# Kernel optimization log

Measured on AMD Instinct MI355X. Metric: run time of the kernel, lower is better.

Reference implementation:

```python
import jax, jax.numpy as jnp
import numpy as np

EPS = 1e-5

def layer_norm(x, gamma, beta):
    mu = jnp.mean(x, axis=-1, keepdims=True)
    var = jnp.mean(jnp.square(x - mu), axis=-1, keepdims=True)
    return (x - mu) * jax.lax.rsqrt(var + EPS) * gamma + beta

def setup_inputs() -> dict:
    key = jax.random.key(0)
    ks = jax.random.split(key, 12)
    B, N, F, H, K = 32, 2048, 128, 256, 64
    A_hat = jax.random.uniform(ks[0], (B, N, N), dtype=jnp.float32) / N  # row-normalized-ish adjacency
    X = jax.random.normal(ks[1], (B, N, F), dtype=jnp.float32)
    def lin(k, din, dout):
        s = 1.0 / np.sqrt(din)
        k1, k2 = jax.random.split(k)
        W = jax.random.uniform(k1, (din, dout), minval=-s, maxval=s, dtype=jnp.float32)
        b = jax.random.uniform(k2, (dout,), minval=-s, maxval=s, dtype=jnp.float32)
        return W, b
    W1, b1 = lin(ks[2], F, H)
    W2, b2 = lin(ks[3], H, H)
    Wa, ba = lin(ks[4], H, K)
    Wl, bl = lin(ks[5], H, K)
    g1 = jnp.ones((H,), jnp.float32); beta1 = jnp.zeros((H,), jnp.float32)
    g2 = jnp.ones((H,), jnp.float32); beta2 = jnp.zeros((H,), jnp.float32)
    return {"A_hat": A_hat, "X": X, "W1": W1, "b1": b1, "g1": g1, "beta1": beta1,
            "W2": W2, "b2": b2, "g2": g2, "beta2": beta2,
            "Wa": Wa, "ba": ba, "Wl": Wl, "bl": bl}

def reference(A_hat, X, W1, b1, g1, beta1, W2, b2, g2, beta2, Wa, ba, Wl, bl):
    # Layer 1: aggregate -> linear -> LayerNorm -> ReLU (dropout is eval identity)
    H = jnp.einsum('bnm,bmf->bnf', A_hat, X)
    H = jnp.einsum('bnf,fh->bnh', H, W1) + b1
    H = jax.nn.relu(layer_norm(H, g1, beta1))
    # Layer 2
    H = jnp.einsum('bnm,bmh->bnh', A_hat, H)
    H = jnp.einsum('bnh,hk->bnk', H, W2) + b2
    H = jax.nn.relu(layer_norm(H, g2, beta2))
    # mean readout over nodes
    g = jnp.mean(H, axis=1)
    pred_arr_reg = g @ Wa + ba
    logits = g @ Wl + bl
    return (pred_arr_reg, logits)
```

## Files before the change

### kernel.cpp

```cpp
#include <hip/hip_runtime.h>
#include <hip/hip_bf16.h>

#define NN 2048

typedef __attribute__((ext_vector_type(4))) float f32x4;
typedef __attribute__((ext_vector_type(8))) short bf16x8;

__device__ __forceinline__ unsigned short f2bf(float f) {
  __hip_bfloat16 h = __float2bfloat16(f);
  return __builtin_bit_cast(unsigned short, h);
}
__device__ __forceinline__ unsigned int pk2(float a, float b) {
  return (unsigned int)f2bf(a) | ((unsigned int)f2bf(b) << 16);
}
__device__ __forceinline__ void gld_lds16(const void* g, void* l) {
  __builtin_amdgcn_global_load_lds(
      (const __attribute__((address_space(1))) unsigned int*)g,
      (__attribute__((address_space(3))) unsigned int*)l, 16, 0, 0);
}

__global__ void k_tr_cvt(const float* __restrict__ src, unsigned short* __restrict__ dst,
                         int R, int C) {
  int b = blockIdx.z;
  src += (size_t)b * R * C;
  dst += (size_t)b * R * C;
  __shared__ float tile[32][33];
  int r0 = blockIdx.x * 32, c0 = blockIdx.y * 32;
  int t = threadIdx.x;
  int r = t >> 3, c4 = (t & 7) << 2;
  float4 v = *(const float4*)(src + (size_t)(r0 + r) * C + c0 + c4);
  tile[r][c4 + 0] = v.x; tile[r][c4 + 1] = v.y; tile[r][c4 + 2] = v.z; tile[r][c4 + 3] = v.w;
  __syncthreads();
  ushort4 o;
  o.x = f2bf(tile[c4 + 0][r]); o.y = f2bf(tile[c4 + 1][r]);
  o.z = f2bf(tile[c4 + 2][r]); o.w = f2bf(tile[c4 + 3][r]);
  *(ushort4*)(dst + (size_t)(c0 + r) * R + r0 + c4) = o;
}

#define AGG_STEP(KT, AREGC, AREGN, CUR)                                        \
  {                                                                            \
    const int kt_ = (KT);                                                      \
    if (kt_ < NKT - 2) {                           \
      const float* p_ = apb + (size_t)(kt_ + 2) * 64;                          \
      _Pragma("unroll") for (int j = 0; j < 4; ++j)                            \
          AREGN[j] = ((const float4*)p_)[j];                                   \
    }                                                                          \
    if (kt_ < NKT - 1) {                                                       \
      _Pragma("unroll") for (int i = 0; i < NF; ++i) {        \
        int jj = i * 512 + t;                                                  \
        int n_ = jj >> 3, s_ = jj & 7, sp_ = s_ ^ (n_ & 7);                    \
        gld_lds16(BTb + (size_t)n_ * NN + (size_t)(kt_ + 1) * 64 + sp_ * 8,    \
                  &Bs[(CUR) ^ 1][(i * 512 + wid * 64) * 8]);                   \
      }                                                                        \
      _Pragma("unroll") for (int i = 0; i < 2; ++i) {     \
        uint4 w_;                                                              \
        w_.x = pk2(AREGC[2 * i].x, AREGC[2 * i].y);                            \
        w_.y = pk2(AREGC[2 * i].z, AREGC[2 * i].w);                            \
        w_.z = pk2(AREGC[2 * i + 1].x, AREGC[2 * i + 1].y);                    \
        w_.w = pk2(AREGC[2 * i + 1].z, AREGC[2 * i + 1].w);                    \
        int s_ = ak * 2 + i, sp_ = s_ ^ (ar & 7);                              \
        *(uint4*)&As[(CUR) ^ 1][(ar * 8 + sp_) * 8] = w_;                      \
      }                                                                        \
    }                                                                          \
    _Pragma("unroll") for (int kh = 0; kh < 2; ++kh) {                         \
      bf16x8 af[4], bfr[NF];                                                   \
      _Pragma("unroll") for (int mi = 0; mi < 4; ++mi) {                       \
        int row = wr * 64 + mi * 16 + lr;                                      \
        int sp_ = (kh * 4 + q) ^ (row & 7);                                    \
        af[mi] = *(const bf16x8*)&As[CUR][(row * 8 + sp_) * 8];                \
      }                                                                        \
      _Pragma("unroll") for (int ni = 0; ni < NF; ++ni) {                      \
        int brow = wc * WN + ni * 16 + lr;                                     \
        int sp_ = (kh * 4 + q) ^ (brow & 7);                                   \
        bfr[ni] = *(const bf16x8*)&Bs[CUR][(brow * 8 + sp_) * 8];              \
      }                                                                        \
      _Pragma("unroll") for (int mi = 0; mi < 4; ++mi)                         \
        _Pragma("unroll") for (int ni = 0; ni < NF; ++ni)                      \
          acc[mi][ni] = __builtin_amdgcn_mfma_f32_16x16x32_bf16(               \
              af[mi], bfr[ni], acc[mi][ni], 0, 0, 0);                          \
    }                                                                          \
    __syncthreads();                                                           \
  }

template <int NCOLS, int MODE>
__global__ __launch_bounds__(512, NCOLS == 128 ? 4 : 2) void k_agg_fused(
    const float* __restrict__ A, const unsigned short* __restrict__ BT,
    const unsigned short* __restrict__ WT, const float* __restrict__ bias,
    const float* __restrict__ gamma, const float* __restrict__ beta,
    unsigned short* __restrict__ HTout, float* __restrict__ gpart) {
  constexpr int WN = NCOLS / 4;
  constexpr int NF = NCOLS / 64;
  constexpr int NKT = NN / 64;
  constexpr int FIN = NCOLS;
  constexpr int NQT = FIN / 64;
  constexpr int NMB = NN / 128;

  __shared__ __align__(16) unsigned short As[2][128 * 64];
  __shared__ __align__(16) unsigned short Bs[2][NCOLS * 64];
  __shared__ float red[2][128][4];

  int L = blockIdx.x + gridDim.x * blockIdx.z;
  int xcd = L & 7, slot = L >> 3;
  int mb = slot % NMB;
  int b = xcd + 8 * (slot / NMB);
  int m0 = mb * 128;

  const float* Ab = A + (size_t)b * NN * NN;
  const unsigned short* BTb = BT + (size_t)b * (size_t)NCOLS * NN;
  int t = threadIdx.x, lane = t & 63, wid = t >> 6;
  int wr = wid >> 2, wc = wid & 3;
  int q = lane >> 4, lr = lane & 15;
  int ar = t >> 2, ak = t & 3;
  const float* apb = Ab + (size_t)(m0 + ar) * NN + ak * 16;

  f32x4 acc[4][NF] = {};
  float4 aregA[4], aregB[4];

  {
#pragma unroll
    for (int j = 0; j < 4; ++j) aregA[j] = ((const float4*)apb)[j];
#pragma unroll
    for (int i = 0; i < NF; ++i) {
      int jj = i * 512 + t;
      int n = jj >> 3, s = jj & 7, sp = s ^ (n & 7);
      gld_lds16(BTb + (size_t)n * NN + sp * 8, &Bs[0][(i * 512 + wid * 64) * 8]);
    }
#pragma unroll
    for (int i = 0; i < 2; ++i) {
      uint4 w;
      w.x = pk2(aregA[2 * i].x, aregA[2 * i].y);
      w.y = pk2(aregA[2 * i].z, aregA[2 * i].w);
      w.z = pk2(aregA[2 * i + 1].x, aregA[2 * i + 1].y);
      w.w = pk2(aregA[2 * i + 1].z, aregA[2 * i + 1].w);
      int s = ak * 2 + i, sp = s ^ (ar & 7);
      *(uint4*)&As[0][(ar * 8 + sp) * 8] = w;
    }
#pragma unroll
    for (int j = 0; j < 4; ++j) aregB[j] = ((const float4*)(apb + 64))[j];
  }
  __syncthreads();

  for (int k2 = 0; k2 < NKT / 2; ++k2) {
    AGG_STEP(2 * k2, aregB, aregA, 0);
    AGG_STEP(2 * k2 + 1, aregA, aregB, 1);
  }

  unsigned short* Hs = (NCOLS == 128) ? &As[0][0] : &Bs[0][0];
  unsigned short* Ws = (NCOLS == 128) ? &Bs[0][0] : &As[0][0];
#pragma unroll
  for (int mi = 0; mi < 4; ++mi) {
#pragma unroll
    for (int ni = 0; ni < NF; ++ni) {
#pragma unroll
      for (int j = 0; j < 4; ++j) {
        int row = wr * 64 + mi * 16 + q * 4 + j;
        int col = wc * WN + ni * 16 + lr;
        int sp = (col >> 3) ^ (row & 7);
        Hs[row * FIN + sp * 8 + (col & 7)] = f2bf(acc[mi][ni][j]);
      }
    }
  }

  f32x4 acc2[4][4] = {};
  for (int qt = 0; qt < NQT; ++qt) {
    __syncthreads();
#pragma unroll
    for (int i = 0; i < 4; ++i) {
      int jj = i * 512 + t;
      int h = jj >> 3, s = jj & 7, sp = s ^ (h & 7);
      gld_lds16(WT + (size_t)h * FIN + qt * 64 + sp * 8, Ws + (i * 512 + wid * 64) * 8);
    }
    __syncthreads();
#pragma unroll
    for (int kh = 0; kh < 2; ++kh) {
      bf16x8 hf[4], wf[4];
#pragma unroll
      for (int mi = 0; mi < 4; ++mi) {
        int row = wr * 64 + mi * 16 + lr;
        int slotk = qt * 8 + kh * 4 + q;
        int sp = slotk ^ (row & 7);
        hf[mi] = *(const bf16x8*)&Hs[row * FIN + sp * 8];
      }
#pragma unroll
      for (int ni = 0; ni < 4; ++ni) {
        int h = wc * 64 + ni * 16 + lr;
        int sp = (kh * 4 + q) ^ (h & 7);
        wf[ni] = *(const bf16x8*)&Ws[(h * 8 + sp) * 8];
      }
#pragma unroll
      for (int mi = 0; mi < 4; ++mi) {
#pragma unroll
        for (int ni = 0; ni < 4; ++ni)
          acc2[mi][ni] = __builtin_amdgcn_mfma_f32_16x16x32_bf16(hf[mi], wf[ni], acc2[mi][ni], 0, 0, 0);
      }
    }
  }

  float bcol[4], gcol[4], zcol[4];
#pragma unroll
  for (int ni = 0; ni < 4; ++ni) {
    int col = wc * 64 + ni * 16 + lr;
    bcol[ni] = bias[col]; gcol[ni] = gamma[col]; zcol[ni] = beta[col];
  }
#pragma unroll
  for (int mi = 0; mi < 4; ++mi) {
#pragma unroll
    for (int j = 0; j < 4; ++j) {
      float s = 0.f, ss = 0.f;
#pragma unroll
      for (int ni = 0; ni < 4; ++ni) {
        float v = acc2[mi][ni][j] + bcol[ni];
        acc2[mi][ni][j] = v;
        s += v; ss += v * v;
      }
#pragma unroll
      for (int m = 1; m < 16; m <<= 1) { s += __shfl_xor(s, m); ss += __shfl_xor(ss, m); }
      if (lr == 0) {
        int rl = wr * 64 + mi * 16 + q * 4 + j;
        red[0][rl][wc] = s;
        red[1][rl][wc] = ss;
      }
    }
  }
  __syncthreads();
#pragma unroll
  for (int mi = 0; mi < 4; ++mi) {
#pragma unroll
    for (int j = 0; j < 4; ++j) {
      int rl = wr * 64 + mi * 16 + q * 4 + j;
      float s = red[0][rl][0] + red[0][rl][1] + red[0][rl][2] + red[0][rl][3];
      float ss = red[1][rl][0] + red[1][rl][1] + red[1][rl][2] + red[1][rl][3];
      float mean = s * (1.f / 256.f);
      float var = ss * (1.f / 256.f) - mean * mean;
      float inv = rsqrtf(var + 1e-5f);
#pragma unroll
      for (int ni = 0; ni < 4; ++ni) {
        float v = (acc2[mi][ni][j] - mean) * inv * gcol[ni] + zcol[ni];
        acc2[mi][ni][j] = v > 0.f ? v : 0.f;
      }
    }
  }
  if (MODE == 0) {
#pragma unroll
    for (int mi = 0; mi < 4; ++mi) {
#pragma unroll
      for (int ni = 0; ni < 4; ++ni) {
        int col = wc * 64 + ni * 16 + lr;
        int rowb = m0 + wr * 64 + mi * 16 + q * 4;
        ushort4 o;
        o.x = f2bf(acc2[mi][ni][0]); o.y = f2bf(acc2[mi][ni][1]);
        o.z = f2bf(acc2[mi][ni][2]); o.w = f2bf(acc2[mi][ni][3]);
        *(ushort4*)(HTout + ((size_t)b * 256 + col) * NN + rowb) = o;
      }
    }
  } else {
#pragma unroll
    for (int ni = 0; ni < 4; ++ni) {
      float cs = 0.f;
#pragma unroll
      for (int mi = 0; mi < 4; ++mi) {
#pragma unroll
        for (int j = 0; j < 4; ++j) cs += acc2[mi][ni][j];
      }
      cs += __shfl_xor(cs, 16);
      cs += __shfl_xor(cs, 32);
      if (q == 0) {
        int col = wc * 64 + ni * 16 + lr;
        gpart[(((size_t)b * NMB + mb) * 2 + wr) * 256 + col] = cs;
      }
    }
  }
}

__global__ void k_readout(const float* __restrict__ gpart, const float* __restrict__ Wa,
                          const float* __restrict__ ba, const float* __restrict__ Wl,
                          const float* __restrict__ bl, float* __restrict__ out) {
  __shared__ float gl[256];
  int b = blockIdx.x, t = threadIdx.x;
  float s = 0.f;
#pragma unroll 4
  for (int p = 0; p < 32; ++p) s += gpart[((size_t)b * 32 + p) * 256 + t];
  gl[t] = s * (1.f / 2048.f);
  __syncthreads();
  if (t < 128) {
    int k = t & 63;
    const float* W = (t >= 64) ? Wl : Wa;
    const float* bb = (t >= 64) ? bl : ba;
    float a = 0.f;
    for (int h = 0; h < 256; ++h) a += gl[h] * W[h * 64 + k];
    a += bb[k];
    out[((t >= 64) ? 2048 : 0) + b * 64 + k] = a;
  }
}

extern "C" void kernel_launch(void* const* d_in, const int* in_sizes, int n_in,
                              void* d_out, int out_size, void* d_ws, size_t ws_size,
                              hipStream_t stream) {
  const float* A_hat = (const float*)d_in[0];
  const float* X   = (const float*)d_in[1];
  const float* W1  = (const float*)d_in[2];
  const float* b1  = (const float*)d_in[3];
  const float* g1  = (const float*)d_in[4];
  const float* be1 = (const float*)d_in[5];
  const float* W2  = (const float*)d_in[6];
  const float* b2  = (const float*)d_in[7];
  const float* g2  = (const float*)d_in[8];
  const float* be2 = (const float*)d_in[9];
  const float* Wa  = (const float*)d_in[10];
  const float* ba  = (const float*)d_in[11];
  const float* Wl  = (const float*)d_in[12];
  const float* bl  = (const float*)d_in[13];

  char* ws = (char*)d_ws;
  const size_t MB = 1024 * 1024;
  unsigned short* XT  = (unsigned short*)(ws);
  unsigned short* H1T = (unsigned short*)(ws + 16 * MB);
  unsigned short* W1T = (unsigned short*)(ws + 48 * MB);
  unsigned short* W2T = (unsigned short*)(ws + 48 * MB + 256 * 1024);
  float* gpart        = (float*)(ws + 49 * MB);

  k_tr_cvt<<<dim3(64, 4, 32), 256, 0, stream>>>(X, XT, 2048, 128);
  k_tr_cvt<<<dim3(4, 8, 1), 256, 0, stream>>>(W1, W1T, 128, 256);
  k_tr_cvt<<<dim3(8, 8, 1), 256, 0, stream>>>(W2, W2T, 256, 256);
  k_agg_fused<128, 0><<<dim3(16, 1, 32), 512, 0, stream>>>(
      A_hat, XT, W1T, b1, g1, be1, H1T, nullptr);
  k_agg_fused<256, 1><<<dim3(16, 1, 32), 512, 0, stream>>>(
      A_hat, H1T, W2T, b2, g2, be2, nullptr, gpart);
  k_readout<<<dim3(32), 256, 0, stream>>>(gpart, Wa, ba, Wl, bl, (float*)d_out);
}
```

Baseline: 332.5 us.

## Coalesce A_hat tile loads and merge transpose-convert launches into one kernel

The fp32 A_hat staging loads are remapped so that 16 consecutive threads read one 256-byte contiguous row segment (four rows per thread, 32 rows apart), instead of each thread reading 64 contiguous bytes. The bf16 writes into shared memory change to 8-byte stores with the same XOR swizzle. Separately, the three transpose-convert launches for X, W1 and W2 become a single kernel with a flat grid, which removes two launches. The aim is better global-memory coalescing on the dominant A_hat stream plus lower launch overhead; the cost is more, smaller LDS stores and more address arithmetic.

```diff
diff --git a/kernel.cpp b/kernel.cpp
--- a/kernel.cpp
+++ b/kernel.cpp
@@ -19,13 +19,31 @@
       (__attribute__((address_space(3))) unsigned int*)l, 16, 0, 0);
 }
 
-__global__ void k_tr_cvt(const float* __restrict__ src, unsigned short* __restrict__ dst,
-                         int R, int C) {
-  int b = blockIdx.z;
+__global__ void k_tr_all(const float* __restrict__ X, unsigned short* __restrict__ XT,
+                         const float* __restrict__ W1, unsigned short* __restrict__ W1T,
+                         const float* __restrict__ W2, unsigned short* __restrict__ W2T) {
+  int bid = blockIdx.x;
+  const float* src;
+  unsigned short* dst;
+  int R, C, bx, by, b;
+  if (bid < 8192) {
+    src = X; dst = XT; R = 2048; C = 128;
+    b = bid >> 8;
+    int r = bid & 255;
+    bx = r & 63; by = r >> 6;
+  } else if (bid < 8192 + 32) {
+    src = W1; dst = W1T; R = 128; C = 256; b = 0;
+    int r = bid - 8192;
+    bx = r & 3; by = r >> 2;
+  } else {
+    src = W2; dst = W2T; R = 256; C = 256; b = 0;
+    int r = bid - 8224;
+    bx = r & 7; by = r >> 3;
+  }
   src += (size_t)b * R * C;
   dst += (size_t)b * R * C;
   __shared__ float tile[32][33];
-  int r0 = blockIdx.x * 32, c0 = blockIdx.y * 32;
+  int r0 = bx * 32, c0 = by * 32;
   int t = threadIdx.x;
   int r = t >> 3, c4 = (t & 7) << 2;
   float4 v = *(const float4*)(src + (size_t)(r0 + r) * C + c0 + c4);
@@ -43,7 +61,7 @@
     if (kt_ < NKT - 2) {                           \
       const float* p_ = apb + (size_t)(kt_ + 2) * 64;                          \
       _Pragma("unroll") for (int j = 0; j < 4; ++j)                            \
-          AREGN[j] = ((const float4*)p_)[j];                                   \
+          AREGN[j] = *(const float4*)(p_ + (size_t)j * 32 * NN);               \
     }                                                                          \
     if (kt_ < NKT - 1) {                                                       \
       _Pragma("unroll") for (int i = 0; i < NF; ++i) {        \
@@ -52,14 +70,13 @@
         gld_lds16(BTb + (size_t)n_ * NN + (size_t)(kt_ + 1) * 64 + sp_ * 8,    \
                   &Bs[(CUR) ^ 1][(i * 512 + wid * 64) * 8]);                   \
       }                                                                        \
-      _Pragma("unroll") for (int i = 0; i < 2; ++i) {     \
-        uint4 w_;                                                              \
-        w_.x = pk2(AREGC[2 * i].x, AREGC[2 * i].y);                            \
-        w_.y = pk2(AREGC[2 * i].z, AREGC[2 * i].w);                            \
-        w_.z = pk2(AREGC[2 * i + 1].x, AREGC[2 * i + 1].y);                    \
-        w_.w = pk2(AREGC[2 * i + 1].z, AREGC[2 * i + 1].w);                    \
-        int s_ = ak * 2 + i, sp_ = s_ ^ (ar & 7);                              \
-        *(uint4*)&As[(CUR) ^ 1][(ar * 8 + sp_) * 8] = w_;                      \
+      _Pragma("unroll") for (int j = 0; j < 4; ++j) {     \
+        uint2 w_;                                                              \
+        w_.x = pk2(AREGC[j].x, AREGC[j].y);                                    \
+        w_.y = pk2(AREGC[j].z, AREGC[j].w);                                    \
+        int row_ = arow + 32 * j;                                              \
+        int sp_ = aslot ^ (row_ & 7);                                          \
+        *(uint2*)&As[(CUR) ^ 1][(row_ * 8 + sp_) * 8 + ahalf * 4] = w_;        \
       }                                                                        \
     }                                                                          \
     _Pragma("unroll") for (int kh = 0; kh < 2; ++kh) {                         \
@@ -110,15 +127,17 @@
   int t = threadIdx.x, lane = t & 63, wid = t >> 6;
   int wr = wid >> 2, wc = wid & 3;
   int q = lane >> 4, lr = lane & 15;
-  int ar = t >> 2, ak = t & 3;
-  const float* apb = Ab + (size_t)(m0 + ar) * NN + ak * 16;
+  int arow = t >> 4;
+  int aslot = (t >> 1) & 7;
+  int ahalf = t & 1;
+  const float* apb = Ab + (size_t)(m0 + arow) * NN + (t & 15) * 4;
 
   f32x4 acc[4][NF] = {};
   float4 aregA[4], aregB[4];
 
   {
 #pragma unroll
-    for (int j = 0; j < 4; ++j) aregA[j] = ((const float4*)apb)[j];
+    for (int j = 0; j < 4; ++j) aregA[j] = *(const float4*)(apb + (size_t)j * 32 * NN);
 #pragma unroll
     for (int i = 0; i < NF; ++i) {
       int jj = i * 512 + t;
@@ -126,17 +145,16 @@
       gld_lds16(BTb + (size_t)n * NN + sp * 8, &Bs[0][(i * 512 + wid * 64) * 8]);
     }
 #pragma unroll
-    for (int i = 0; i < 2; ++i) {
-      uint4 w;
-      w.x = pk2(aregA[2 * i].x, aregA[2 * i].y);
-      w.y = pk2(aregA[2 * i].z, aregA[2 * i].w);
-      w.z = pk2(aregA[2 * i + 1].x, aregA[2 * i + 1].y);
-      w.w = pk2(aregA[2 * i + 1].z, aregA[2 * i + 1].w);
-      int s = ak * 2 + i, sp = s ^ (ar & 7);
-      *(uint4*)&As[0][(ar * 8 + sp) * 8] = w;
-    }
-#pragma unroll
-    for (int j = 0; j < 4; ++j) aregB[j] = ((const float4*)(apb + 64))[j];
+    for (int j = 0; j < 4; ++j) {
+      uint2 w;
+      w.x = pk2(aregA[j].x, aregA[j].y);
+      w.y = pk2(aregA[j].z, aregA[j].w);
+      int row_ = arow + 32 * j;
+      int sp = aslot ^ (row_ & 7);
+      *(uint2*)&As[0][(row_ * 8 + sp) * 8 + ahalf * 4] = w;
+    }
+#pragma unroll
+    for (int j = 0; j < 4; ++j) aregB[j] = *(const float4*)(apb + 64 + (size_t)j * 32 * NN);
   }
   __syncthreads();
 
@@ -319,9 +337,7 @@
   unsigned short* W2T = (unsigned short*)(ws + 48 * MB + 256 * 1024);
   float* gpart        = (float*)(ws + 49 * MB);
 
-  k_tr_cvt<<<dim3(64, 4, 32), 256, 0, stream>>>(X, XT, 2048, 128);
-  k_tr_cvt<<<dim3(4, 8, 1), 256, 0, stream>>>(W1, W1T, 128, 256);
-  k_tr_cvt<<<dim3(8, 8, 1), 256, 0, stream>>>(W2, W2T, 256, 256);
+  k_tr_all<<<dim3(8288), 256, 0, stream>>>(X, XT, W1, W1T, W2, W2T);
   k_agg_fused<128, 0><<<dim3(16, 1, 32), 512, 0, stream>>>(
       A_hat, XT, W1T, b1, g1, be1, H1T, nullptr);
   k_agg_fused<256, 1><<<dim3(16, 1, 32), 512, 0, stream>>>(
```

Measured after the change: 344.9 us. 1.04x slower.

## Merge transpose launches and replace syncthreads with partial vmcnt waits in GEMM loop

Applied to the files above, without the earlier changes.

Combines the three transpose/convert kernels into one launch that dispatches by block index, removing two kernel launches. In the aggregation main loop, the LDS-direct B loads are issued before the A register prefetch, and the full __syncthreads is replaced by an explicit waitcnt that leaves the 4 outstanding A-prefetch global loads in flight, followed by s_barrier. The last two steps are peeled so they drain with vmcnt(0). This lets the next tile's A global loads overlap with the barrier, but it relies on exact counting of outstanding memory operations for correctness.

```diff
diff --git a/kernel.cpp b/kernel.cpp
--- a/kernel.cpp
+++ b/kernel.cpp
@@ -19,13 +19,31 @@
       (__attribute__((address_space(3))) unsigned int*)l, 16, 0, 0);
 }
 
-__global__ void k_tr_cvt(const float* __restrict__ src, unsigned short* __restrict__ dst,
-                         int R, int C) {
-  int b = blockIdx.z;
+__global__ void k_tr_all(const float* __restrict__ X, unsigned short* __restrict__ XT,
+                         const float* __restrict__ W1, unsigned short* __restrict__ W1T,
+                         const float* __restrict__ W2, unsigned short* __restrict__ W2T) {
+  int bid = blockIdx.x;
+  const float* src;
+  unsigned short* dst;
+  int R, C, bx, by, b;
+  if (bid < 8192) {
+    src = X; dst = XT; R = 2048; C = 128;
+    b = bid >> 8;
+    int r = bid & 255;
+    bx = r & 63; by = r >> 6;
+  } else if (bid < 8192 + 32) {
+    src = W1; dst = W1T; R = 128; C = 256; b = 0;
+    int r = bid - 8192;
+    bx = r & 3; by = r >> 2;
+  } else {
+    src = W2; dst = W2T; R = 256; C = 256; b = 0;
+    int r = bid - 8224;
+    bx = r & 7; by = r >> 3;
+  }
   src += (size_t)b * R * C;
   dst += (size_t)b * R * C;
   __shared__ float tile[32][33];
-  int r0 = blockIdx.x * 32, c0 = blockIdx.y * 32;
+  int r0 = bx * 32, c0 = by * 32;
   int t = threadIdx.x;
   int r = t >> 3, c4 = (t & 7) << 2;
   float4 v = *(const float4*)(src + (size_t)(r0 + r) * C + c0 + c4);
@@ -37,22 +55,25 @@
   *(ushort4*)(dst + (size_t)(c0 + r) * R + r0 + c4) = o;
 }
 
-#define AGG_STEP(KT, AREGC, AREGN, CUR)                                        \
+#define AGG_STEP(KT, AREGC, AREGN, CUR, VMC)                                   \
   {                                                                            \
     const int kt_ = (KT);                                                      \
-    if (kt_ < NKT - 2) {                           \
-      const float* p_ = apb + (size_t)(kt_ + 2) * 64;                          \
-      _Pragma("unroll") for (int j = 0; j < 4; ++j)                            \
-          AREGN[j] = ((const float4*)p_)[j];                                   \
-    }                                                                          \
-    if (kt_ < NKT - 1) {                                                       \
-      _Pragma("unroll") for (int i = 0; i < NF; ++i) {        \
+    if (kt_ < NKT - 1) {    \
+      _Pragma("unroll") for (int i = 0; i < NF; ++i) {                         \
         int jj = i * 512 + t;                                                  \
         int n_ = jj >> 3, s_ = jj & 7, sp_ = s_ ^ (n_ & 7);                    \
         gld_lds16(BTb + (size_t)n_ * NN + (size_t)(kt_ + 1) * 64 + sp_ * 8,    \
                   &Bs[(CUR) ^ 1][(i * 512 + wid * 64) * 8]);                   \
       }                                                                        \
-      _Pragma("unroll") for (int i = 0; i < 2; ++i) {     \
+    }                                                                          \
+    __builtin_amdgcn_sched_barrier(0);      \
+    if (kt_ < NKT - 2) {    \
+      const float* p_ = apb + (size_t)(kt_ + 2) * 64;                          \
+      _Pragma("unroll") for (int j = 0; j < 4; ++j)                            \
+          AREGN[j] = ((const float4*)p_)[j];                                   \
+    }                                                                          \
+    if (kt_ < NKT - 1) {    \
+      _Pragma("unroll") for (int i = 0; i < 2; ++i) {                          \
         uint4 w_;                                                              \
         w_.x = pk2(AREGC[2 * i].x, AREGC[2 * i].y);                            \
         w_.y = pk2(AREGC[2 * i].z, AREGC[2 * i].w);                            \
@@ -79,7 +100,8 @@
           acc[mi][ni] = __builtin_amdgcn_mfma_f32_16x16x32_bf16(               \
               af[mi], bfr[ni], acc[mi][ni], 0, 0, 0);                          \
     }                                                                          \
-    __syncthreads();                                                           \
+    asm volatile("s_waitcnt vmcnt(" #VMC ") lgkmcnt(0)" ::: "memory");         \
+    __builtin_amdgcn_s_barrier();                                              \
   }
 
 template <int NCOLS, int MODE>
@@ -135,15 +157,19 @@
       int s = ak * 2 + i, sp = s ^ (ar & 7);
       *(uint4*)&As[0][(ar * 8 + sp) * 8] = w;
     }
+    __builtin_amdgcn_sched_barrier(0);
 #pragma unroll
     for (int j = 0; j < 4; ++j) aregB[j] = ((const float4*)(apb + 64))[j];
-  }
-  __syncthreads();
-
-  for (int k2 = 0; k2 < NKT / 2; ++k2) {
-    AGG_STEP(2 * k2, aregB, aregA, 0);
-    AGG_STEP(2 * k2 + 1, aregA, aregB, 1);
-  }
+    asm volatile("s_waitcnt vmcnt(4) lgkmcnt(0)" ::: "memory");
+    __builtin_amdgcn_s_barrier();
+  }
+
+  for (int k2 = 0; k2 < NKT / 2 - 1; ++k2) {
+    AGG_STEP(2 * k2, aregB, aregA, 0, 4);
+    AGG_STEP(2 * k2 + 1, aregA, aregB, 1, 4);
+  }
+  AGG_STEP(NKT - 2, aregB, aregA, 0, 0);
+  AGG_STEP(NKT - 1, aregA, aregB, 1, 0);
 
   unsigned short* Hs = (NCOLS == 128) ? &As[0][0] : &Bs[0][0];
   unsigned short* Ws = (NCOLS == 128) ? &Bs[0][0] : &As[0][0];
@@ -319,9 +345,7 @@
   unsigned short* W2T = (unsigned short*)(ws + 48 * MB + 256 * 1024);
   float* gpart        = (float*)(ws + 49 * MB);
 
-  k_tr_cvt<<<dim3(64, 4, 32), 256, 0, stream>>>(X, XT, 2048, 128);
-  k_tr_cvt<<<dim3(4, 8, 1), 256, 0, stream>>>(W1, W1T, 128, 256);
-  k_tr_cvt<<<dim3(8, 8, 1), 256, 0, stream>>>(W2, W2T, 256, 256);
+  k_tr_all<<<dim3(8288), 256, 0, stream>>>(X, XT, W1, W1T, W2, W2T);
   k_agg_fused<128, 0><<<dim3(16, 1, 32), 512, 0, stream>>>(
       A_hat, XT, W1T, b1, g1, be1, H1T, nullptr);
   k_agg_fused<256, 1><<<dim3(16, 1, 32), 512, 0, stream>>>(
```

After: 322.8 us. 1.03x faster.
